# Optimization experiments

Measured on AMD Instinct MI355X. Metric: run time of the kernel, lower is better.

## Reference

```python
import jax, jax.numpy as jnp
import numpy as np

B, S, E, H, D, F = 384, 128, 512, 4, 128, 2048

def setup_inputs() -> dict:
    key = jax.random.key(0)
    ks = jax.random.split(key, 13)
    lecun = lambda k, fan_in, shape: jax.random.normal(k, shape, jnp.float32) / jnp.sqrt(fan_in)
    return {
        "x": jax.random.normal(ks[0], (B, S, E), jnp.float32),
        "wq": lecun(ks[1], E, (E, E)), "bq": jnp.zeros((E,), jnp.float32),
        "wk": lecun(ks[2], E, (E, E)), "bk": jnp.zeros((E,), jnp.float32),
        "wv": lecun(ks[3], E, (E, E)), "bv": jnp.zeros((E,), jnp.float32),
        "wo": lecun(ks[4], E, (E, E)), "bo": jnp.zeros((E,), jnp.float32),
        "w1": lecun(ks[5], E, (E, F)), "b1": jnp.zeros((F,), jnp.float32),
        "w2": lecun(ks[6], F, (F, E)), "b2": jnp.zeros((E,), jnp.float32),
    }

def reference(x, wq, bq, wk, bk, wv, bv, wo, bo, w1, b1, w2, b2):
    # Attention (no 1/sqrt(d) scaling, no causal mask — matches source)
    q = (x @ wq + bq).reshape(B, S, H, D)
    k = (x @ wk + bk).reshape(B, S, H, D)
    v = (x @ wv + bv).reshape(B, S, H, D)
    scores = jnp.einsum('bshd,bthd->bhst', q, k)  # [B,H,S,S]
    weights = jax.nn.softmax(scores, axis=-1)
    attn = jnp.einsum('bhst,bthd->bshd', weights, v).reshape(B, S, E)
    x = x + (attn @ wo + bo)
    # MLP with residual
    h = jax.nn.relu(x @ w1 + b1)
    x = x + (h @ w2 + b2)
    return x
```

## Files before the change

### kernel.cpp

```cpp
#include <hip/hip_runtime.h>
#include <hip/hip_bf16.h>
#include <stdint.h>

typedef unsigned short u16;
typedef _Float16 f16;
typedef __attribute__((ext_vector_type(8))) f16 f16x8;
typedef __attribute__((ext_vector_type(4))) float f32x4;
typedef __attribute__((ext_vector_type(8))) u16 u16x8;

__device__ __forceinline__ u16 f2h(float f) {
    return __builtin_bit_cast(u16, (f16)f);
}
__device__ __forceinline__ float h2f(u16 u) {
    return (float)__builtin_bit_cast(f16, u);
}

#define GLDS16(g, l) __builtin_amdgcn_global_load_lds( \
    (const __attribute__((address_space(1))) void*)(uintptr_t)(g), \
    (__attribute__((address_space(3))) void*)(uintptr_t)(l), 16, 0, 0)

__global__ __launch_bounds__(256) void transpose_w(
    const float* __restrict__ in, u16* __restrict__ out,
    int K, int N, int rowOff)
{
    __shared__ float tile[32][33];
    int n0 = blockIdx.x * 32;
    int k0 = blockIdx.y * 32;
    int tx = threadIdx.x & 31;
    int ty = threadIdx.x >> 5;
#pragma unroll
    for (int i = 0; i < 4; ++i) {
        int k = ty + i * 8;
        tile[k][tx] = in[(size_t)(k0 + k) * N + n0 + tx];
    }
    __syncthreads();
#pragma unroll
    for (int i = 0; i < 4; ++i) {
        int n = ty + i * 8;
        out[(size_t)(rowOff + n0 + n) * K + k0 + tx] = f2h(tile[tx][n]);
    }
}

__global__ __launch_bounds__(256) void transpose_w4(
    const float* __restrict__ wq, const float* __restrict__ wk,
    const float* __restrict__ wv, const float* __restrict__ wo,
    u16* __restrict__ wqkvT, u16* __restrict__ woT)
{
    __shared__ float tile[32][33];
    const float* src[4] = {wq, wk, wv, wo};
    const int z = blockIdx.z;
    const float* in = src[z];
    u16* out = (z == 3) ? woT : (wqkvT + (size_t)z * 512 * 512);
    int n0 = blockIdx.x * 32;
    int k0 = blockIdx.y * 32;
    int tx = threadIdx.x & 31;
    int ty = threadIdx.x >> 5;
#pragma unroll
    for (int i = 0; i < 4; ++i) {
        int k = ty + i * 8;
        tile[k][tx] = in[(size_t)(k0 + k) * 512 + n0 + tx];
    }
    __syncthreads();
#pragma unroll
    for (int i = 0; i < 4; ++i) {
        int n = ty + i * 8;
        out[(size_t)(n0 + n) * 512 + k0 + tx] = f2h(tile[tx][n]);
    }
}

__global__ void pack_bias3(const float* __restrict__ bq, const float* __restrict__ bk,
                           const float* __restrict__ bv, float* __restrict__ bqkv)
{
    int i = blockIdx.x * 256 + threadIdx.x;
    float v;
    if (i < 512) v = bq[i];
    else if (i < 1024) v = bk[i - 512];
    else v = bv[i - 1024];
    bqkv[i] = v;
}

__global__ __launch_bounds__(256) void convert_x(const float* __restrict__ in,
                                                 u16* __restrict__ out)
{
    size_t i = ((size_t)blockIdx.x * 256 + threadIdx.x) * 8;
    float4 a = *(const float4*)(in + i);
    float4 b = *(const float4*)(in + i + 4);
    u16x8 r;
    r[0] = f2h(a.x); r[1] = f2h(a.y); r[2] = f2h(a.z); r[3] = f2h(a.w);
    r[4] = f2h(b.x); r[5] = f2h(b.y); r[6] = f2h(b.z); r[7] = f2h(b.w);
    *(u16x8*)(out + i) = r;
}

template<int RES, bool RELU, bool WH, bool WF32>
__global__ __launch_bounds__(256, 2) void gemm_bt(
    const u16* __restrict__ A, int lda,
    const u16* __restrict__ BT, int ldb,
    const float* __restrict__ bias, const void* __restrict__ res,
    u16* __restrict__ outh, float* __restrict__ outf,
    int nb_n, int N, int K)
{
    __shared__ u16 As[128 * 64];
    __shared__ u16 Bs[128 * 64];
    const int tid  = threadIdx.x;
    const int lane = tid & 63;
    const int wv   = tid >> 6;
    const int nwg  = gridDim.x;
    const int cpx  = nwg >> 3;
    const int logical = (blockIdx.x & 7) * cpx + (blockIdx.x >> 3);
    const int m0   = (logical / nb_n) * 128;
    const int n0   = (logical % nb_n) * 128;
    const int wm   = (wv >> 1) * 64;
    const int wn   = (wv & 1) * 64;
    const int lhi  = lane >> 4;
    const int llo  = lane & 15;

    f32x4 acc[4][4] = {};

    for (int kt = 0; kt < K; kt += 64) {
        __syncthreads();
#pragma unroll
        for (int i = 0; i < 4; ++i) {
            int c = i * 256 + tid;
            int row = c >> 3;
            int chunk = (c & 7) ^ (row & 7);
            const u16* ga = A  + (size_t)(m0 + row) * lda + kt + chunk * 8;
            const u16* gb = BT + (size_t)(n0 + row) * ldb + kt + chunk * 8;
            char* la = (char*)As + ((i * 256 + wv * 64) << 4);
            char* lb = (char*)Bs + ((i * 256 + wv * 64) << 4);
            GLDS16(ga, la);
            GLDS16(gb, lb);
        }
        __syncthreads();
#pragma unroll
        for (int fk = 0; fk < 2; ++fk) {
            f16x8 af[4], bfr[4];
#pragma unroll
            for (int f = 0; f < 4; ++f) {
                int ra = wm + f * 16 + llo;
                af[f] = *(const f16x8*)((const char*)As +
                        ((ra << 7) + ((fk * 64 + (lhi << 4)) ^ ((ra & 7) << 4))));
                int rb = wn + f * 16 + llo;
                bfr[f] = *(const f16x8*)((const char*)Bs +
                        ((rb << 7) + ((fk * 64 + (lhi << 4)) ^ ((rb & 7) << 4))));
            }
#pragma unroll
            for (int fm = 0; fm < 4; ++fm)
#pragma unroll
                for (int fn = 0; fn < 4; ++fn)
                    acc[fm][fn] = __builtin_amdgcn_mfma_f32_16x16x32_f16(
                        af[fm], bfr[fn], acc[fm][fn], 0, 0, 0);
        }
    }

    const int cr = lhi * 4;
#pragma unroll
    for (int fm = 0; fm < 4; ++fm) {
#pragma unroll
        for (int fn = 0; fn < 4; ++fn) {
            const int col = n0 + wn + fn * 16 + llo;
            const float bia = bias[col];
#pragma unroll
            for (int r = 0; r < 4; ++r) {
                const int row = m0 + wm + fm * 16 + cr + r;
                float v = acc[fm][fn][r] + bia;
                if constexpr (RES == 2) v += h2f(((const u16*)res)[(size_t)row * N + col]);
                if constexpr (RELU) v = fmaxf(v, 0.f);
                if constexpr (WF32) outf[(size_t)row * N + col] = v;
                if constexpr (WH)   outh[(size_t)row * N + col] = f2h(v);
            }
        }
    }
}

__global__ __launch_bounds__(256, 2) void attn_kernel(
    const u16* __restrict__ qkv, u16* __restrict__ attn)
{
    __shared__ u16 VT[128 * 128];
    __shared__ u16 Plds[4 * 32 * 128];
    const int tid  = threadIdx.x;
    const int lane = tid & 63;
    const int wv   = tid >> 6;
    const int b    = blockIdx.x >> 2;
    const int hh   = blockIdx.x & 3;
    const int lhi  = lane >> 4;
    const int llo  = lane & 15;
    const u16* base = qkv + (size_t)b * 128 * 1536;

#pragma unroll
    for (int i = 0; i < 8; ++i) {
        int c = i * 256 + tid;
        int t = c >> 4;
        int ch = c & 15;
        uint4 raw = *(const uint4*)(base + (size_t)t * 1536 + 1024 + hh * 128 + ch * 8);
        const u16* e = (const u16*)&raw;
#pragma unroll
        for (int j = 0; j < 8; ++j) {
            int d = ch * 8 + j;
            *(u16*)((char*)VT + ((d << 8) + ((t * 2) ^ ((d & 7) << 4)))) = e[j];
        }
    }

    f16x8 qf[2][4];
#pragma unroll
    for (int fm = 0; fm < 2; ++fm)
#pragma unroll
        for (int fk = 0; fk < 4; ++fk) {
            int srow = wv * 32 + fm * 16 + llo;
            qf[fm][fk] = *(const f16x8*)(base + (size_t)srow * 1536 + hh * 128 + fk * 32 + lhi * 8);
        }

    f32x4 acc[2][8] = {};
#pragma unroll
    for (int ft = 0; ft < 8; ++ft) {
        f16x8 kf[4];
#pragma unroll
        for (int fk = 0; fk < 4; ++fk) {
            int trow = ft * 16 + llo;
            kf[fk] = *(const f16x8*)(base + (size_t)trow * 1536 + 512 + hh * 128 + fk * 32 + lhi * 8);
        }
#pragma unroll
        for (int fm = 0; fm < 2; ++fm)
#pragma unroll
            for (int fk = 0; fk < 4; ++fk)
                acc[fm][ft] = __builtin_amdgcn_mfma_f32_16x16x32_f16(
                    qf[fm][fk], kf[fk], acc[fm][ft], 0, 0, 0);
    }

    float inv[2][4];
#pragma unroll
    for (int fm = 0; fm < 2; ++fm)
#pragma unroll
        for (int r = 0; r < 4; ++r) {
            float mx = acc[fm][0][r];
#pragma unroll
            for (int ft = 1; ft < 8; ++ft) mx = fmaxf(mx, acc[fm][ft][r]);
            mx = fmaxf(mx, __shfl_xor(mx, 1, 64));
            mx = fmaxf(mx, __shfl_xor(mx, 2, 64));
            mx = fmaxf(mx, __shfl_xor(mx, 4, 64));
            mx = fmaxf(mx, __shfl_xor(mx, 8, 64));
            float s = 0.f;
#pragma unroll
            for (int ft = 0; ft < 8; ++ft) {
                float p = __expf(acc[fm][ft][r] - mx);
                acc[fm][ft][r] = p;
                s += p;
            }
            s += __shfl_xor(s, 1, 64);
            s += __shfl_xor(s, 2, 64);
            s += __shfl_xor(s, 4, 64);
            s += __shfl_xor(s, 8, 64);
            inv[fm][r] = 1.f / s;
        }

    char* Pw = (char*)Plds + wv * 8192;
#pragma unroll
    for (int fm = 0; fm < 2; ++fm)
#pragma unroll
        for (int ft = 0; ft < 8; ++ft)
#pragma unroll
            for (int r = 0; r < 4; ++r) {
                int m = fm * 16 + lhi * 4 + r;
                int t = ft * 16 + llo;
                *(u16*)(Pw + ((m << 8) + ((t * 2) ^ ((m & 7) << 4)))) = f2h(acc[fm][ft][r]);
            }

    __syncthreads();

    f16x8 pf[2][4];
#pragma unroll
    for (int fm = 0; fm < 2; ++fm)
#pragma unroll
        for (int k2 = 0; k2 < 4; ++k2) {
            int m = fm * 16 + llo;
            pf[fm][k2] = *(const f16x8*)(Pw +
                ((m << 8) + ((k2 * 64 + (lhi << 4)) ^ ((m & 7) << 4))));
        }

    f32x4 o[2][8] = {};
#pragma unroll
    for (int fd = 0; fd < 8; ++fd) {
        f16x8 vf[4];
#pragma unroll
        for (int k2 = 0; k2 < 4; ++k2) {
            int d = fd * 16 + llo;
            vf[k2] = *(const f16x8*)((const char*)VT +
                ((d << 8) + ((k2 * 64 + (lhi << 4)) ^ ((d & 7) << 4))));
        }
#pragma unroll
        for (int fm = 0; fm < 2; ++fm)
#pragma unroll
            for (int k2 = 0; k2 < 4; ++k2)
                o[fm][fd] = __builtin_amdgcn_mfma_f32_16x16x32_f16(
                    pf[fm][k2], vf[k2], o[fm][fd], 0, 0, 0);
    }

#pragma unroll
    for (int fm = 0; fm < 2; ++fm)
#pragma unroll
        for (int fd = 0; fd < 8; ++fd)
#pragma unroll
            for (int r = 0; r < 4; ++r) {
                int row = b * 128 + wv * 32 + fm * 16 + lhi * 4 + r;
                int col = hh * 128 + fd * 16 + llo;
                attn[(size_t)row * 512 + col] = f2h(o[fm][fd][r] * inv[fm][r]);
            }
}

extern "C" void kernel_launch(void* const* d_in, const int* in_sizes, int n_in,
                              void* d_out, int out_size, void* d_ws, size_t ws_size,
                              hipStream_t stream)
{
    const float* x  = (const float*)d_in[0];
    const float* wq = (const float*)d_in[1];
    const float* bq = (const float*)d_in[2];
    const float* wk = (const float*)d_in[3];
    const float* bk = (const float*)d_in[4];
    const float* wv = (const float*)d_in[5];
    const float* bv = (const float*)d_in[6];
    const float* wo = (const float*)d_in[7];
    const float* bo = (const float*)d_in[8];
    const float* w1 = (const float*)d_in[9];
    const float* b1 = (const float*)d_in[10];
    const float* w2 = (const float*)d_in[11];
    const float* b2 = (const float*)d_in[12];
    float* out = (float*)d_out;

    char* ws = (char*)d_ws;
    u16*   wqkvT = (u16*)(ws + 0);
    u16*   woT   = (u16*)(ws + 1572864);
    u16*   w1T   = (u16*)(ws + 2097152);
    u16*   w2T   = (u16*)(ws + 4194304);
    float* bqkv  = (float*)(ws + 6291456);
    u16*   xf    = (u16*)(ws + 6297600);
    u16*   qkv   = (u16*)(ws + 56629248);
    u16*   attno = (u16*)(ws + 207624192);
    u16*   x1h   = xf;
    u16*   hbuf  = qkv;

    transpose_w4<<<dim3(16, 16, 4), 256, 0, stream>>>(wq, wk, wv, wo, wqkvT, woT);
    transpose_w<<<dim3(64, 16), 256, 0, stream>>>(w1, w1T, 512, 2048, 0);
    transpose_w<<<dim3(16, 64), 256, 0, stream>>>(w2, w2T, 2048, 512, 0);
    pack_bias3<<<6, 256, 0, stream>>>(bq, bk, bv, bqkv);
    convert_x<<<12288, 256, 0, stream>>>(x, xf);

    gemm_bt<0, false, true, false><<<4608, 256, 0, stream>>>(
        xf, 512, wqkvT, 512, bqkv, nullptr, qkv, nullptr, 12, 1536, 512);
    attn_kernel<<<1536, 256, 0, stream>>>(qkv, attno);
    gemm_bt<2, false, true, false><<<1536, 256, 0, stream>>>(
        attno, 512, woT, 512, bo, xf, x1h, nullptr, 4, 512, 512);
    gemm_bt<0, true, true, false><<<6144, 256, 0, stream>>>(
        x1h, 512, w1T, 512, b1, nullptr, hbuf, nullptr, 16, 2048, 512);
    gemm_bt<2, false, false, true><<<1536, 256, 0, stream>>>(
        hbuf, 2048, w2T, 2048, b2, x1h, nullptr, out, 4, 512, 2048);
}
```

Before: 442.5 us.

## Fuse fp32-to-fp16 input conversion and bias packing into QKV GEMM

Removes the separate convert_x and pack_bias3 kernels. A new QKV GEMM loads fp32 x tiles straight into LDS and converts them to fp16 in registers before the MFMA. It also picks the q, k or v bias per column block. The output-projection residual now reads the original fp32 x, which drops the fp16 x copy and its extra global write and read. In exchange the A tile in LDS doubles in size, which may lower occupancy or LDS bandwidth per MFMA and adds conversion ALU work inside the inner loop.

Measured after the change: 499.8 us. +13.0%, slower.

```diff
diff --git a/kernel.cpp b/kernel.cpp
--- a/kernel.cpp
+++ b/kernel.cpp
@@ -68,27 +68,100 @@
     }
 }
 
-__global__ void pack_bias3(const float* __restrict__ bq, const float* __restrict__ bk,
-                           const float* __restrict__ bv, float* __restrict__ bqkv)
-{
-    int i = blockIdx.x * 256 + threadIdx.x;
-    float v;
-    if (i < 512) v = bq[i];
-    else if (i < 1024) v = bk[i - 512];
-    else v = bv[i - 1024];
-    bqkv[i] = v;
-}
-
-__global__ __launch_bounds__(256) void convert_x(const float* __restrict__ in,
-                                                 u16* __restrict__ out)
-{
-    size_t i = ((size_t)blockIdx.x * 256 + threadIdx.x) * 8;
-    float4 a = *(const float4*)(in + i);
-    float4 b = *(const float4*)(in + i + 4);
-    u16x8 r;
-    r[0] = f2h(a.x); r[1] = f2h(a.y); r[2] = f2h(a.z); r[3] = f2h(a.w);
-    r[4] = f2h(b.x); r[5] = f2h(b.y); r[6] = f2h(b.z); r[7] = f2h(b.w);
-    *(u16x8*)(out + i) = r;
+__global__ __launch_bounds__(256, 2) void gemm_qkv(
+    const float* __restrict__ X,
+    const u16* __restrict__ BT,
+    const float* __restrict__ bq, const float* __restrict__ bk,
+    const float* __restrict__ bv,
+    u16* __restrict__ outh, int nb_n, int N)
+{
+    __shared__ float Af[128 * 64];
+    __shared__ u16   Bs[128 * 64];
+    const int tid  = threadIdx.x;
+    const int lane = tid & 63;
+    const int wv   = tid >> 6;
+    const int nwg  = gridDim.x;
+    const int cpx  = nwg >> 3;
+    const int logical = (blockIdx.x & 7) * cpx + (blockIdx.x >> 3);
+    const int m0   = (logical / nb_n) * 128;
+    const int n0   = (logical % nb_n) * 128;
+    const int wm   = (wv >> 1) * 64;
+    const int wn   = (wv & 1) * 64;
+    const int lhi  = lane >> 4;
+    const int llo  = lane & 15;
+
+    f32x4 acc[4][4] = {};
+
+    for (int kt = 0; kt < 512; kt += 64) {
+        __syncthreads();
+#pragma unroll
+        for (int i = 0; i < 8; ++i) {
+            int c = i * 256 + tid;
+            int row = c >> 4;
+            int sl = (c & 15) ^ (row & 7);
+            const float* ga = X + (size_t)(m0 + row) * 512 + kt + sl * 4;
+            char* la = (char*)Af + ((i * 256 + wv * 64) << 4);
+            GLDS16(ga, la);
+        }
+#pragma unroll
+        for (int i = 0; i < 4; ++i) {
+            int c = i * 256 + tid;
+            int row = c >> 3;
+            int chunk = (c & 7) ^ (row & 7);
+            const u16* gb = BT + (size_t)(n0 + row) * 512 + kt + chunk * 8;
+            char* lb = (char*)Bs + ((i * 256 + wv * 64) << 4);
+            GLDS16(gb, lb);
+        }
+        __syncthreads();
+#pragma unroll
+        for (int fk = 0; fk < 2; ++fk) {
+            f16x8 af[4], bfr[4];
+#pragma unroll
+            for (int f = 0; f < 4; ++f) {
+                int ra = wm + f * 16 + llo;
+                int bo = fk * 128 + lhi * 32;
+                int sxa = (ra & 7) << 4;
+                f32x4 a0 = *(const f32x4*)((const char*)Af +
+                            ((ra << 8) + (bo ^ sxa)));
+                f32x4 a1 = *(const f32x4*)((const char*)Af +
+                            ((ra << 8) + ((bo + 16) ^ sxa)));
+#pragma unroll
+                for (int j = 0; j < 4; ++j) {
+                    af[f][j]     = (f16)a0[j];
+                    af[f][j + 4] = (f16)a1[j];
+                }
+                int rb = wn + f * 16 + llo;
+                bfr[f] = *(const f16x8*)((const char*)Bs +
+                        ((rb << 7) + ((fk * 64 + (lhi << 4)) ^ ((rb & 7) << 4))));
+            }
+#pragma unroll
+            for (int fm = 0; fm < 4; ++fm)
+#pragma unroll
+                for (int fn = 0; fn < 4; ++fn)
+                    acc[fm][fn] = __builtin_amdgcn_mfma_f32_16x16x32_f16(
+                        af[fm], bfr[fn], acc[fm][fn], 0, 0, 0);
+        }
+    }
+
+    const float* bptr; int cbase;
+    if (n0 < 512)       { bptr = bq; cbase = 0; }
+    else if (n0 < 1024) { bptr = bk; cbase = 512; }
+    else                { bptr = bv; cbase = 1024; }
+
+    const int cr = lhi * 4;
+#pragma unroll
+    for (int fm = 0; fm < 4; ++fm) {
+#pragma unroll
+        for (int fn = 0; fn < 4; ++fn) {
+            const int col = n0 + wn + fn * 16 + llo;
+            const float bia = bptr[col - cbase];
+#pragma unroll
+            for (int r = 0; r < 4; ++r) {
+                const int row = m0 + wm + fm * 16 + cr + r;
+                outh[(size_t)row * N + col] = f2h(acc[fm][fn][r] + bia);
+            }
+        }
+    }
 }
 
 template<int RES, bool RELU, bool WH, bool WF32>
@@ -163,6 +236,7 @@
             for (int r = 0; r < 4; ++r) {
                 const int row = m0 + wm + fm * 16 + cr + r;
                 float v = acc[fm][fn][r] + bia;
+                if constexpr (RES == 1) v += ((const float*)res)[(size_t)row * N + col];
                 if constexpr (RES == 2) v += h2f(((const u16*)res)[(size_t)row * N + col]);
                 if constexpr (RELU) v = fmaxf(v, 0.f);
                 if constexpr (WF32) outf[(size_t)row * N + col] = v;
@@ -330,24 +404,20 @@
     u16*   woT   = (u16*)(ws + 1572864);
     u16*   w1T   = (u16*)(ws + 2097152);
     u16*   w2T   = (u16*)(ws + 4194304);
-    float* bqkv  = (float*)(ws + 6291456);
-    u16*   xf    = (u16*)(ws + 6297600);
+    u16*   x1h   = (u16*)(ws + 6297600);
     u16*   qkv   = (u16*)(ws + 56629248);
     u16*   attno = (u16*)(ws + 207624192);
-    u16*   x1h   = xf;
     u16*   hbuf  = qkv;
 
     transpose_w4<<<dim3(16, 16, 4), 256, 0, stream>>>(wq, wk, wv, wo, wqkvT, woT);
     transpose_w<<<dim3(64, 16), 256, 0, stream>>>(w1, w1T, 512, 2048, 0);
     transpose_w<<<dim3(16, 64), 256, 0, stream>>>(w2, w2T, 2048, 512, 0);
-    pack_bias3<<<6, 256, 0, stream>>>(bq, bk, bv, bqkv);
-    convert_x<<<12288, 256, 0, stream>>>(x, xf);
-
-    gemm_bt<0, false, true, false><<<4608, 256, 0, stream>>>(
-        xf, 512, wqkvT, 512, bqkv, nullptr, qkv, nullptr, 12, 1536, 512);
+
+    gemm_qkv<<<4608, 256, 0, stream>>>(
+        x, wqkvT, bq, bk, bv, qkv, 12, 1536);
     attn_kernel<<<1536, 256, 0, stream>>>(qkv, attno);
-    gemm_bt<2, false, true, false><<<1536, 256, 0, stream>>>(
-        attno, 512, woT, 512, bo, xf, x1h, nullptr, 4, 512, 512);
+    gemm_bt<1, false, true, false><<<1536, 256, 0, stream>>>(
+        attno, 512, woT, 512, bo, x, x1h, nullptr, 4, 512, 512);
     gemm_bt<0, true, true, false><<<6144, 256, 0, stream>>>(
         x1h, 512, w1T, 512, b1, nullptr, hbuf, nullptr, 16, 2048, 512);
     gemm_bt<2, false, false, true><<<1536, 256, 0, stream>>>(
```
